# Kernel optimization log

Hardware: AMD Instinct MI355X
Metric: run time of the kernel (lower is better)

## Reference

```python
import jax, jax.numpy as jnp
import numpy as np


def setup_inputs() -> dict:
    key = jax.random.key(0)
    k1, k2 = jax.random.split(key)
    x = jax.random.normal(k1, (4, 64, 32, 64, 64), dtype=jnp.float32)
    # Conv3d(2, 1, kernel_size=7, padding=3, bias=False) weight: [out_c=1, in_c=2, 7, 7, 7]
    conv_w = jax.random.normal(k2, (1, 2, 7, 7, 7), dtype=jnp.float32) * 0.05
    return {"x": x, "conv_w": conv_w}


def reference(x, conv_w):
    # x: [B, C, D, H, W]
    avg_out = jnp.mean(x, axis=1, keepdims=True)          # [B,1,D,H,W]
    max_out = jnp.max(x, axis=1, keepdims=True)           # [B,1,D,H,W]
    pooled = jnp.concatenate([avg_out, max_out], axis=1)  # [B,2,D,H,W]
    att = jax.lax.conv_general_dilated(
        pooled, conv_w,
        window_strides=(1, 1, 1),
        padding=[(3, 3), (3, 3), (3, 3)],
        dimension_numbers=("NCDHW", "OIDHW", "NCDHW"),
    )  # [B,1,D,H,W]
    att = jax.nn.sigmoid(att)
    return x * att
```

## Files before the change

### kernel.cpp

```cpp
#include <hip/hip_runtime.h>
#include <math.h>

#define BB 4
#define CC 64
#define DD 32
#define HH 64
#define WW 64
#define DHW (DD * HH * WW)
#define NP  (BB * DHW)
#define CDHW (CC * DHW)
#define TOTAL (BB * CDHW)

__global__ void pool_kernel(const float* __restrict__ x,
                            float* __restrict__ out) {
    int tid4 = blockIdx.x * blockDim.x + threadIdx.x;
    int i = tid4 * 4;
    int b = i >> 17;
    int s = i & (DHW - 1);
    const float* base = x + (size_t)b * CDHW + s;
    float4 v = *(const float4*)base;
    float4 sum = v, mx = v;
#pragma unroll 8
    for (int c = 1; c < CC; ++c) {
        float4 u = *(const float4*)(base + (size_t)c * DHW);
        sum.x += u.x; sum.y += u.y; sum.z += u.z; sum.w += u.w;
        mx.x = fmaxf(mx.x, u.x); mx.y = fmaxf(mx.y, u.y);
        mx.z = fmaxf(mx.z, u.z); mx.w = fmaxf(mx.w, u.w);
    }
    const float inv = 1.0f / (float)CC;
    float4 av; av.x = sum.x * inv; av.y = sum.y * inv;
    av.z = sum.z * inv; av.w = sum.w * inv;
    *(float4*)(out + (size_t)b * CDHW + 1 * DHW + s) = av;
    *(float4*)(out + (size_t)b * CDHW + 2 * DHW + s) = mx;
}

__global__ void conv_kernel(const float* __restrict__ cw,
                            float* __restrict__ out) {
    __shared__ float wsm[2 * 343];
    for (int idx = threadIdx.x; idx < 686; idx += 256)
        wsm[idx] = cw[idx];
    __syncthreads();

    int bx = blockIdx.x;
    int hblk = bx & 3;
    int d = (bx >> 2) & 31;
    int b = bx >> 7;
    int tid = threadIdx.x;
    int wg = tid & 15;
    int h = (hblk << 4) + (tid >> 4);
    int w0 = wg << 2;

    float acc0 = 0.f, acc1 = 0.f, acc2 = 0.f, acc3 = 0.f;

    for (int ch = 0; ch < 2; ++ch) {
        const float* plane = out + (size_t)b * CDHW + (size_t)(ch + 1) * DHW;
        const float* wch = wsm + ch * 343;
#pragma unroll
        for (int kd = 0; kd < 7; ++kd) {
            int dd = d + kd - 3;
            if (dd < 0 || dd >= DD) continue;
#pragma unroll
            for (int kh = 0; kh < 7; ++kh) {
                int hh = h + kh - 3;
                if (hh < 0 || hh >= HH) continue;
                const float* row = plane + ((dd << 6) + hh) * WW;
                float vals[10];
#pragma unroll
                for (int t = 0; t < 10; ++t) {
                    int ww = w0 - 3 + t;
                    vals[t] = (ww >= 0 && ww < WW) ? row[ww] : 0.f;
                }
                const float* wrow = wch + (kd * 7 + kh) * 7;
#pragma unroll
                for (int kw = 0; kw < 7; ++kw) {
                    float wv = wrow[kw];
                    acc0 = fmaf(vals[kw + 0], wv, acc0);
                    acc1 = fmaf(vals[kw + 1], wv, acc1);
                    acc2 = fmaf(vals[kw + 2], wv, acc2);
                    acc3 = fmaf(vals[kw + 3], wv, acc3);
                }
            }
        }
    }

    size_t o = (size_t)b * CDHW + (size_t)((d << 6) + h) * WW + w0;
    out[o + 0] = 1.f / (1.f + __expf(-acc0));
    out[o + 1] = 1.f / (1.f + __expf(-acc1));
    out[o + 2] = 1.f / (1.f + __expf(-acc2));
    out[o + 3] = 1.f / (1.f + __expf(-acc3));
}

__global__ void scale_kernel(const float* __restrict__ x,
                             float* __restrict__ out) {
    int tid4 = blockIdx.x * blockDim.x + threadIdx.x;
    int i = tid4 * 4;
    int b = i >> 17;
    int s = i & (DHW - 1);
    size_t base = (size_t)b * CDHW + s;
    float4 av = *(const float4*)(out + base);
#pragma unroll 4
    for (int c = 0; c < CC; ++c) {
        float4 xv = *(const float4*)(x + base + (size_t)c * DHW);
        float4 o;
        o.x = xv.x * av.x; o.y = xv.y * av.y;
        o.z = xv.z * av.z; o.w = xv.w * av.w;
        *(float4*)(out + base + (size_t)c * DHW) = o;
    }
}

extern "C" void kernel_launch(void* const* d_in, const int* in_sizes, int n_in,
                              void* d_out, int out_size, void* d_ws, size_t ws_size,
                              hipStream_t stream) {
    const float* x  = (const float*)d_in[0];
    const float* cw = (const float*)d_in[1];
    float* out = (float*)d_out;

    pool_kernel<<<NP / 4 / 256, 256, 0, stream>>>(x, out);
    conv_kernel<<<BB * DD * (HH / 16), 256, 0, stream>>>(cw, out);
    scale_kernel<<<NP / 4 / 256, 256, 0, stream>>>(x, out);
}
```

Baseline: 341.3 us.

## Stage conv input planes in per-wave LDS with double-buffered prefetch

The 7x7x7 conv now loads each depth plane's halo tile (10 rows x 72 cols) into per-wavefront LDS with float4 loads, and prefetches the next plane into registers while computing the current one. Weights are read straight from global memory instead of being staged in shared memory, and the output is stored as a float4. The aim is to replace many scalar, bounds-checked global loads with coalesced vector loads and LDS reuse. This relies on wave-synchronous execution with no __syncthreads, and the total runtime is dominated by the pool and scale kernels.

```diff
diff --git a/kernel.cpp b/kernel.cpp
--- a/kernel.cpp
+++ b/kernel.cpp
@@ -9,7 +9,6 @@
 #define DHW (DD * HH * WW)
 #define NP  (BB * DHW)
 #define CDHW (CC * DHW)
-#define TOTAL (BB * CDHW)
 
 __global__ void pool_kernel(const float* __restrict__ x,
                             float* __restrict__ out) {
@@ -34,60 +33,103 @@
     *(float4*)(out + (size_t)b * CDHW + 2 * DHW + s) = mx;
 }
 
-__global__ void conv_kernel(const float* __restrict__ cw,
-                            float* __restrict__ out) {
-    __shared__ float wsm[2 * 343];
-    for (int idx = threadIdx.x; idx < 686; idx += 256)
-        wsm[idx] = cw[idx];
-    __syncthreads();
+#define ROWF 76
+#define PLANEF (10 * ROWF)
+
+__global__ __launch_bounds__(256) void conv_kernel(const float* __restrict__ cw,
+                                                   float* __restrict__ out) {
+    __shared__ float lds[4 * 2 * PLANEF];
 
     int bx = blockIdx.x;
     int hblk = bx & 3;
     int d = (bx >> 2) & 31;
     int b = bx >> 7;
     int tid = threadIdx.x;
-    int wg = tid & 15;
-    int h = (hblk << 4) + (tid >> 4);
+    int wv = tid >> 6, lane = tid & 63;
+    int wg = lane & 15, hl = lane >> 4;
+    int h0w = (hblk << 4) + (wv << 2);
+    int h = h0w + hl;
     int w0 = wg << 2;
 
+    float* region = lds + wv * (2 * PLANEF);
+
+    int roff[3], goff[3]; bool okhc[3]; bool act[3];
+#pragma unroll
+    for (int j = 0; j < 3; ++j) {
+        int k = lane + 64 * j;
+        int r = k / 18, c = k - r * 18;
+        int hh = h0w - 3 + r;
+        act[j]  = (k < 180);
+        okhc[j] = act[j] && (hh >= 0) && (hh < HH) && (c >= 1) && (c <= 16);
+        roff[j] = r * ROWF + (c << 2);
+        goff[j] = (hh << 6) + (c << 2) - 4;
+    }
+
+    const float* outb = out + (size_t)b * CDHW;
     float acc0 = 0.f, acc1 = 0.f, acc2 = 0.f, acc3 = 0.f;
 
-    for (int ch = 0; ch < 2; ++ch) {
-        const float* plane = out + (size_t)b * CDHW + (size_t)(ch + 1) * DHW;
-        const float* wch = wsm + ch * 343;
+    auto load_plane = [&](int p, float4* st) {
+        int ch = (p >= 7) ? 1 : 0;
+        int kd = p - ch * 7;
+        int dd = d + kd - 3;
+        bool dok = (dd >= 0) && (dd < DD);
+        const float* pb = outb + (size_t)(ch + 1) * DHW + ((size_t)dd << 12);
 #pragma unroll
-        for (int kd = 0; kd < 7; ++kd) {
-            int dd = d + kd - 3;
-            if (dd < 0 || dd >= DD) continue;
+        for (int j = 0; j < 3; ++j) {
+            float4 v = make_float4(0.f, 0.f, 0.f, 0.f);
+            if (dok && okhc[j]) v = *(const float4*)(pb + goff[j]);
+            st[j] = v;
+        }
+    };
+    auto write_plane = [&](float* buf, const float4* st) {
 #pragma unroll
-            for (int kh = 0; kh < 7; ++kh) {
-                int hh = h + kh - 3;
-                if (hh < 0 || hh >= HH) continue;
-                const float* row = plane + ((dd << 6) + hh) * WW;
-                float vals[10];
+        for (int j = 0; j < 3; ++j)
+            if (act[j]) *(float4*)(buf + roff[j]) = st[j];
+    };
+    auto compute_plane = [&](const float* buf, int p) {
+        int ch = (p >= 7) ? 1 : 0;
+        int kd = p - ch * 7;
+        const float* wp = cw + ch * 343 + kd * 49;
 #pragma unroll
-                for (int t = 0; t < 10; ++t) {
-                    int ww = w0 - 3 + t;
-                    vals[t] = (ww >= 0 && ww < WW) ? row[ww] : 0.f;
-                }
-                const float* wrow = wch + (kd * 7 + kh) * 7;
+        for (int kh = 0; kh < 7; ++kh) {
+            const float* rp = buf + (hl + kh) * ROWF + w0;
+            float4 q0 = *(const float4*)(rp);
+            float4 q1 = *(const float4*)(rp + 4);
+            float4 q2 = *(const float4*)(rp + 8);
+            float a[12] = {q0.x, q0.y, q0.z, q0.w,
+                           q1.x, q1.y, q1.z, q1.w,
+                           q2.x, q2.y, q2.z, q2.w};
+            const float* wr = wp + kh * 7;
 #pragma unroll
-                for (int kw = 0; kw < 7; ++kw) {
-                    float wv = wrow[kw];
-                    acc0 = fmaf(vals[kw + 0], wv, acc0);
-                    acc1 = fmaf(vals[kw + 1], wv, acc1);
-                    acc2 = fmaf(vals[kw + 2], wv, acc2);
-                    acc3 = fmaf(vals[kw + 3], wv, acc3);
-                }
+            for (int kw = 0; kw < 7; ++kw) {
+                float wvv = wr[kw];
+                acc0 = fmaf(a[kw + 1], wvv, acc0);
+                acc1 = fmaf(a[kw + 2], wvv, acc1);
+                acc2 = fmaf(a[kw + 3], wvv, acc2);
+                acc3 = fmaf(a[kw + 4], wvv, acc3);
             }
         }
+    };
+
+    float4 st[3];
+    load_plane(0, st);
+    write_plane(region, st);
+    for (int p = 0; p < 14; ++p) {
+        float* cur = region + (p & 1) * PLANEF;
+        float* nxt = region + ((p + 1) & 1) * PLANEF;
+        float4 nx[3];
+        if (p < 13) load_plane(p + 1, nx);
+        compute_plane(cur, p);
+        if (p < 13) write_plane(nxt, nx);
     }
 
     size_t o = (size_t)b * CDHW + (size_t)((d << 6) + h) * WW + w0;
-    out[o + 0] = 1.f / (1.f + __expf(-acc0));
-    out[o + 1] = 1.f / (1.f + __expf(-acc1));
-    out[o + 2] = 1.f / (1.f + __expf(-acc2));
-    out[o + 3] = 1.f / (1.f + __expf(-acc3));
+    float4 r;
+    r.x = 1.f / (1.f + __expf(-acc0));
+    r.y = 1.f / (1.f + __expf(-acc1));
+    r.z = 1.f / (1.f + __expf(-acc2));
+    r.w = 1.f / (1.f + __expf(-acc3));
+    *(float4*)(out + o) = r;
 }
 
 __global__ void scale_kernel(const float* __restrict__ x,
```

New measurement: 291.7 us. 1.17x faster.
